# Optimization experiments

Hardware: AMD Instinct MI355X
Metric: run time of the kernel (lower is better)

## Reference

```python
import jax, jax.numpy as jnp
import numpy as np

B, D, H, W = 8, 128, 152, 272
N_DET = 128
NHEAD = 8
DFF = 512


def _vis_pos_table(d):
    # PositionEmbeddingSine over the fixed 11-entry visibility grid [0,0.1,...,1.0]
    x_embed = jnp.arange(11, dtype=jnp.float32) * 0.1
    dim_t = jnp.arange(d, dtype=jnp.float32)
    dim_t = 10000.0 ** (2.0 * jnp.floor(dim_t / 2.0) / d)
    pos = x_embed[:, None] / dim_t  # [11, d]
    return jnp.stack([jnp.sin(pos[:, 0::2]), jnp.cos(pos[:, 1::2])], axis=2).reshape(11, d)


def _layer_norm(x, g, b, eps=1e-5):
    m = jnp.mean(x, axis=-1, keepdims=True)
    v = jnp.var(x, axis=-1, keepdims=True)
    return (x - m) / jnp.sqrt(v + eps) * g + b


def _adaptive_pool3(x, dets):
    # Faithful AdaptiveAvgPool2d(3) over per-detection crops, vectorized via integral image.
    # x: [B,D,H,W]; dets: [B,N,4] int boxes [x0,y0,x1,y1] with x1>x0, y1>y0.
    P = jnp.cumsum(jnp.cumsum(x, axis=2), axis=3)
    P = jnp.pad(P, ((0, 0), (0, 0), (1, 0), (1, 0)))  # [B,D,H+1,W+1]
    Pt = P.transpose(0, 2, 3, 1)  # [B,H+1,W+1,D]
    sx, sy, ex, ey = dets[..., 0], dets[..., 1], dets[..., 2], dets[..., 3]
    i = jnp.arange(3)

    def edges(s, e):
        # torch adaptive pool bins: start = floor(i*L/3), end = ceil((i+1)*L/3)
        L = (e - s)[..., None]
        st = s[..., None] + (i * L) // 3
        en = s[..., None] + -((-(i + 1) * L) // 3)
        return st, en

    ys, ye = edges(sy, ey)  # [B,N,3]
    xs, xe = edges(sx, ex)
    bidx = jnp.arange(x.shape[0])[:, None, None, None]
    Y0 = ys[:, :, :, None]; Y1 = ye[:, :, :, None]
    X0 = xs[:, :, None, :]; X1 = xe[:, :, None, :]
    g = lambda yy, xx: Pt[bidx, yy, xx]  # [B,N,3,3,D]
    s_ = g(Y1, X1) - g(Y0, X1) - g(Y1, X0) + g(Y0, X0)
    area = ((Y1 - Y0) * (X1 - X0)).astype(x.dtype)  # [B,N,3,3]
    return s_ / area[..., None]  # [B,N,3,3,D] (row-major y,x like .view(128,-1))


def setup_inputs() -> dict:
    key = jax.random.key(0)
    ks = jax.random.split(key, 12)
    x = jax.random.normal(ks[0], (B, D, H, W), jnp.float32)
    vis = jax.random.uniform(ks[1], (B, 1, H, W), jnp.float32)
    # boxes with guaranteed positive extents inside the clamp range (x<=271, y<=151)
    x0 = jax.random.randint(ks[2], (B, N_DET), 0, 230)
    y0 = jax.random.randint(ks[3], (B, N_DET), 0, 110)
    bw = jax.random.randint(ks[4], (B, N_DET), 3, 41)
    bh = jax.random.randint(ks[5], (B, N_DET), 3, 41)
    dets = jnp.stack([x0, y0, x0 + bw, y0 + bh], axis=-1).astype(jnp.int32)
    inds = jax.vmap(lambda k: jax.random.permutation(k, H * W)[:N_DET])(
        jax.random.split(ks[6], B)).astype(jnp.int32)
    s = 1.0 / np.sqrt(D).astype(np.float32)
    Wqkv = jax.random.normal(ks[7], (3 * D, D), jnp.float32) * s
    bqkv = jnp.zeros((3 * D,), jnp.float32)
    Wo = jax.random.normal(ks[8], (D, D), jnp.float32) * s
    bo = jnp.zeros((D,), jnp.float32)
    W1 = jax.random.normal(ks[9], (DFF, D), jnp.float32) * s
    b1 = jnp.zeros((DFF,), jnp.float32)
    W2 = jax.random.normal(ks[10], (D, DFF), jnp.float32) * np.float32(1.0 / np.sqrt(DFF))
    b2 = jnp.zeros((D,), jnp.float32)
    g2 = jnp.ones((D,), jnp.float32); be2 = jnp.zeros((D,), jnp.float32)
    g3 = jnp.ones((D,), jnp.float32); be3 = jnp.zeros((D,), jnp.float32)
    return dict(x=x, vis=vis, dets=dets, inds=inds, Wqkv=Wqkv, bqkv=bqkv, Wo=Wo, bo=bo,
                W1=W1, b1=b1, W2=W2, b2=b2, g2=g2, be2=be2, g3=g3, be3=be3)


def reference(x, vis, dets, inds, Wqkv, bqkv, Wo, bo, W1, b1, W2, b2, g2, be2, g3, be3):
    b, d, h, w = x.shape
    n = inds.shape[1]
    hd = d // NHEAD
    vis_pos = _vis_pos_table(d)  # [11, d]
    # --- query patches: gather point features at detection centers ---
    x_flat = x.transpose(0, 2, 3, 1).reshape(b, h * w, d)
    bidx = jnp.arange(b)[:, None]
    q = x_flat[bidx, inds]  # [b,n,d]
    vis_flat = vis.transpose(0, 2, 3, 1).reshape(b, h * w)
    vidx = (jax.lax.stop_gradient(vis_flat[bidx, inds]) * 10.0).astype(jnp.int32)  # [b,n] in [0,10]
    q = q + vis_pos[vidx]
    # --- key patches: 3x3 adaptive avg pool of each detection crop -> 9 tokens ---
    k = _adaptive_pool3(x, dets).reshape(b * n, 9, d)  # [bn,9,d]
    qf = q.reshape(b * n, 1, d)
    # --- nn.MultiheadAttention cross-attn: batch=b*n detections, L=1 query, S=9 keys ---
    Wq, Wk, Wv = Wqkv[:d], Wqkv[d:2 * d], Wqkv[2 * d:]
    bq, bk, bv = bqkv[:d], bqkv[d:2 * d], bqkv[2 * d:]
    qp = (qf @ Wq.T + bq).reshape(b * n, 1, NHEAD, hd)
    kp = (k @ Wk.T + bk).reshape(b * n, 9, NHEAD, hd)
    vp = (k @ Wv.T + bv).reshape(b * n, 9, NHEAD, hd)
    att = jnp.einsum('blhe,bshe->bhls', qp, kp) / jnp.sqrt(jnp.asarray(hd, x.dtype))
    att = jax.nn.softmax(att, axis=-1)
    ao = jnp.einsum('bhls,bshe->blhe', att, vp).reshape(b * n, 1, d)
    ao = ao @ Wo.T + bo
    # --- post-norm decoder layer (dropout=identity in eval) ---
    t = _layer_norm(qf + ao, g2, be2)
    t2 = jax.nn.relu(t @ W1.T + b1) @ W2.T + b2
    out = _layer_norm(t + t2, g3, be3).reshape(b, n, d)
    # --- scatter refined embeddings back into the feature map ---
    x_flat = x_flat.at[bidx, inds].set(out)
    return x_flat.reshape(b, h, w, d).transpose(0, 3, 1, 2)
```

## Files before the change

kernel.cpp:

```cpp
#include <hip/hip_runtime.h>
#include <math.h>

#define BB 8
#define CH 128
#define HH 152
#define WWID 272
#define HWSZ (HH*WWID)
#define NDET 128
#define NHEAD 8
#define HDIM 16
#define DFF 512
#define NDB (BB*NDET)
#define NPLANE (BB*CH)
#define KSTRIDE 1152
#define CHUNK 19
#define SROW 276

typedef float f4v __attribute__((ext_vector_type(4)));

__device__ __forceinline__ float dot4(float4 w, float4 u, float s) {
    s = fmaf(w.x, u.x, s);
    s = fmaf(w.y, u.y, s);
    s = fmaf(w.z, u.z, s);
    s = fmaf(w.w, u.w, s);
    return s;
}

__global__ __launch_bounds__(256) void pool_stream(
    const float* __restrict__ x, const int* __restrict__ dets,
    float* __restrict__ kout, float* __restrict__ out)
{
    const int bid  = blockIdx.x;
    const int t    = threadIdx.x;
    const int b    = bid >> 7, ch = bid & 127;
    const int lane = t & 63,  w  = t >> 6;

    __shared__ float S[CHUNK * SROW];
    __shared__ float scratch[NDET * 9];

    const float* xp = x + ((size_t)b * CH + ch) * HWSZ;
    f4v* o4 = (f4v*)(out + ((size_t)b * CH + ch) * HWSZ);

    const int d = t & 127, half = t >> 7;
    const int4 dv = *((const int4*)(dets + (size_t)(b * NDET + d) * 4));
    const int sx = dv.x, sy = dv.y, ex = dv.z, ey = dv.w;
    const int Lx = ex - sx, Ly = ey - sy;
    const int xs1 = sx + Lx / 3,        xs2 = sx + 2 * Lx / 3;
    const int xe0 = sx + (Lx + 2) / 3,  xe1 = sx + (2 * Lx + 2) / 3;
    const int ys1 = sy + Ly / 3,        ys2 = sy + 2 * Ly / 3;
    const int ye0 = sy + (Ly + 2) / 3,  ye1 = sy + (2 * Ly + 2) / 3;

    float acc[9] = {0.f,0.f,0.f,0.f,0.f,0.f,0.f,0.f,0.f};

    #pragma unroll 1
    for (int c = 0; c < HH / CHUNK; ++c) {
        const int cbeg = c * CHUNK;

        {
            int rl = w;
            f4v vm = (f4v)(0.f), ve = (f4v)(0.f);
            bool have = (rl < CHUNK);
            if (have) {
                const f4v* rowp = (const f4v*)(xp + (size_t)(cbeg + rl) * WWID);
                vm = rowp[lane];
                if (lane < 4) ve = rowp[64 + lane];
            }
            while (have) {
                const int rc = rl;
                f4v v = vm, e = ve;
                rl += 4;
                have = (rl < CHUNK);
                if (have) {
                    const f4v* rowp = (const f4v*)(xp + (size_t)(cbeg + rl) * WWID);
                    vm = rowp[lane];
                    if (lane < 4) ve = rowp[64 + lane];
                }
                __builtin_nontemporal_store(v, &o4[(size_t)(cbeg + rc) * 68 + lane]);
                if (lane < 4)
                    __builtin_nontemporal_store(e, &o4[(size_t)(cbeg + rc) * 68 + 64 + lane]);
                float T = v[0] + v[1] + v[2] + v[3];
                float s = T;
                #pragma unroll
                for (int o = 1; o < 64; o <<= 1) {
                    float u = __shfl_up(s, o);
                    if (lane >= o) s += u;
                }
                float off0 = s - T;
                float* Sr = S + rc * SROW;
                f4v sm;
                sm[0] = off0;
                sm[1] = off0 + v[0];
                sm[2] = off0 + v[0] + v[1];
                sm[3] = off0 + v[0] + v[1] + v[2];
                *(f4v*)&Sr[4 * lane] = sm;
                float R  = __shfl(s, 63);
                float Te = (lane < 4) ? (e[0]+e[1]+e[2]+e[3]) : 0.f;
                float T0 = __shfl(Te, 0), T1 = __shfl(Te, 1);
                float T2 = __shfl(Te, 2), T3 = __shfl(Te, 3);
                if (lane < 4) {
                    float offE = R + ((lane > 0) ? T0 : 0.f)
                                   + ((lane > 1) ? T1 : 0.f)
                                   + ((lane > 2) ? T2 : 0.f);
                    f4v se;
                    se[0] = offE;
                    se[1] = offE + e[0];
                    se[2] = offE + e[0] + e[1];
                    se[3] = offE + e[0] + e[1] + e[2];
                    *(f4v*)&Sr[256 + 4 * lane] = se;
                }
                if (lane == 0) Sr[272] = R + T0 + T1 + T2 + T3;
            }
        }
        __syncthreads();

        {
            int lo = (sy > cbeg) ? sy : cbeg;
            int hi = (ey < cbeg + CHUNK) ? ey : (cbeg + CHUNK);
            if (lo < hi) {
                int mid = (lo + hi + 1) >> 1;
                int y0 = half ? mid : lo;
                int y1 = half ? hi  : mid;
                for (int y = y0; y < y1; ++y) {
                    const float* Sr = S + (y - cbeg) * SROW;
                    float c0 = Sr[xe0] - Sr[sx];
                    float c1 = Sr[xe1] - Sr[xs1];
                    float c2 = Sr[ex]  - Sr[xs2];
                    float m0 = (y < ye0) ? 1.f : 0.f;
                    float m1 = (y >= ys1 && y < ye1) ? 1.f : 0.f;
                    float m2 = (y >= ys2) ? 1.f : 0.f;
                    acc[0] = fmaf(m0, c0, acc[0]); acc[1] = fmaf(m0, c1, acc[1]); acc[2] = fmaf(m0, c2, acc[2]);
                    acc[3] = fmaf(m1, c0, acc[3]); acc[4] = fmaf(m1, c1, acc[4]); acc[5] = fmaf(m1, c2, acc[5]);
                    acc[6] = fmaf(m2, c0, acc[6]); acc[7] = fmaf(m2, c1, acc[7]); acc[8] = fmaf(m2, c2, acc[8]);
                }
            }
        }
        __syncthreads();
    }

    if (half) {
        #pragma unroll
        for (int j = 0; j < 9; ++j) scratch[d * 9 + j] = acc[j];
    }
    __syncthreads();
    if (!half) {
        const float w0 = (float)(xe0 - sx), w1 = (float)(xe1 - xs1), w2 = (float)(ex - xs2);
        const float h0 = (float)(ye0 - sy), h1r = (float)(ye1 - ys1), h2 = (float)(ey - ys2);
        float aj[9];
        #pragma unroll
        for (int j = 0; j < 9; ++j) aj[j] = acc[j] + scratch[d * 9 + j];
        float* kd = kout + (size_t)(b * NDET + d) * KSTRIDE + ch;
        kd[0*CH] = aj[0] / (h0  * w0);
        kd[1*CH] = aj[1] / (h0  * w1);
        kd[2*CH] = aj[2] / (h0  * w2);
        kd[3*CH] = aj[3] / (h1r * w0);
        kd[4*CH] = aj[4] / (h1r * w1);
        kd[5*CH] = aj[5] / (h1r * w2);
        kd[6*CH] = aj[6] / (h2  * w0);
        kd[7*CH] = aj[7] / (h2  * w1);
        kd[8*CH] = aj[8] / (h2  * w2);
    }
}

#define K2_KV 512
#define K2_Q  64
__global__ __launch_bounds__(256) void qkv_kernel(
    const float* __restrict__ x, const float* __restrict__ vis,
    const int* __restrict__ inds, const float* __restrict__ kout,
    const float* __restrict__ Wqkv, const float* __restrict__ bqkv,
    float* __restrict__ kvp, float* __restrict__ qpb, float* __restrict__ qvb)
{
    const int bid = blockIdx.x;
    const int t   = threadIdx.x;

    __shared__ float As[2304];

    if (bid < K2_KV) {
        const int d0 = bid * 2;
        const float4* src = (const float4*)(kout + (size_t)d0 * KSTRIDE);
        for (int i = t; i < 576; i += 256) ((float4*)As)[i] = src[i];
        __syncthreads();

        const int o = t & 127, which = t >> 7;
        const float4* wr = (const float4*)(Wqkv + (size_t)(CH + which * CH + o) * CH);
        float acc[18];
        #pragma unroll
        for (int r = 0; r < 18; ++r) acc[r] = 0.f;
        for (int i = 0; i < 32; ++i) {
            float4 w = wr[i];
            #pragma unroll
            for (int r = 0; r < 18; ++r) {
                float4 a = ((const float4*)(As + r * 128))[i];
                acc[r] = dot4(w, a, acc[r]);
            }
        }
        const float bias = bqkv[CH + which * CH + o];
        #pragma unroll
        for (int r = 0; r < 18; ++r) {
            int det = d0 + (r / 9), slot = r % 9;
            kvp[(((size_t)det * 2 + which) * 9 + slot) * CH + o] = acc[r] + bias;
        }
    } else {
        const int dg = (bid - K2_KV) * 16;
        const int o  = t & 127;
        const int rh = t >> 7;
        const float fr = powf(10000.0f, -(float)(o & 126) * (1.0f / 128.0f));
        for (int j = 0; j < 8; ++j) {
            int r = rh + 2 * j;
            int det = dg + r;
            int b = det >> 7, n = det & 127;
            int p = inds[b * NDET + n];
            float qval = x[((size_t)b * CH + o) * HWSZ + p];
            float vv   = vis[(size_t)b * HWSZ + p];
            int vidx   = (int)(vv * 10.0f);
            float ang  = 0.1f * (float)vidx * fr;
            float pe   = (o & 1) ? cosf(ang) : sinf(ang);
            float q = qval + pe;
            As[r * 128 + o] = q;
            qvb[(size_t)det * CH + o] = q;
        }
        __syncthreads();
        const float4* wr = (const float4*)(Wqkv + (size_t)o * CH);
        float acc[8] = {0.f,0.f,0.f,0.f,0.f,0.f,0.f,0.f};
        for (int i = 0; i < 32; ++i) {
            float4 w = wr[i];
            #pragma unroll
            for (int j = 0; j < 8; ++j) {
                float4 a = ((const float4*)(As + (rh + 2 * j) * 128))[i];
                acc[j] = dot4(w, a, acc[j]);
            }
        }
        const float bias = bqkv[o];
        #pragma unroll
        for (int j = 0; j < 8; ++j)
            qpb[(size_t)(dg + rh + 2 * j) * CH + o] = acc[j] + bias;
    }
}

__global__ __launch_bounds__(64) void attn_kernel(
    const float* __restrict__ kvp, const float* __restrict__ qpb,
    float* __restrict__ aovb)
{
    const int bid = blockIdx.x;
    const int t   = threadIdx.x;

    __shared__ float qpl[CH];
    __shared__ float kpl[9][CH];
    __shared__ float vpl[9][CH];
    __shared__ float attl[NHEAD][9];

    const int det = bid;
    const float4* kph = (const float4*)(kvp + (size_t)det * 2 * 9 * CH);
    for (int i = t; i < 288; i += 64) ((float4*)kpl)[i] = kph[i];
    for (int i = t; i < 288; i += 64) ((float4*)vpl)[i] = kph[288 + i];
    for (int i = t; i < 32;  i += 64) ((float4*)qpl)[i] = ((const float4*)(qpb + (size_t)det * CH))[i];
    __syncthreads();

    for (int pr = t; pr < NHEAD * 9; pr += 64) {
        int h = pr / 9, s = pr - h * 9;
        const float* qh = qpl + h * HDIM;
        const float* kh = &kpl[s][h * HDIM];
        float a = 0.f;
        #pragma unroll
        for (int e = 0; e < HDIM; ++e) a = fmaf(qh[e], kh[e], a);
        attl[h][s] = a * 0.25f;
    }
    __syncthreads();

    if (t < NHEAD) {
        float m = attl[t][0];
        #pragma unroll
        for (int s = 1; s < 9; ++s) m = fmaxf(m, attl[t][s]);
        float e[9]; float sum = 0.f;
        #pragma unroll
        for (int s = 0; s < 9; ++s) { e[s] = expf(attl[t][s] - m); sum += e[s]; }
        float inv = 1.0f / sum;
        #pragma unroll
        for (int s = 0; s < 9; ++s) attl[t][s] = e[s] * inv;
    }
    __syncthreads();

    for (int o = t; o < CH; o += 64) {
        int h = o >> 4;
        float a = 0.f;
        #pragma unroll
        for (int s = 0; s < 9; ++s) a = fmaf(attl[h][s], vpl[s][o], a);
        aovb[(size_t)det * CH + o] = a;
    }
}

__global__ __launch_bounds__(256) void wo_ln1_ffn1_kernel(
    const float* __restrict__ aovb, const float* __restrict__ qvb,
    const float* __restrict__ Wo, const float* __restrict__ bo,
    const float* __restrict__ g2, const float* __restrict__ be2,
    const float* __restrict__ W1, const float* __restrict__ b1,
    float* __restrict__ tvb, float* __restrict__ h1b)
{
    const int bid = blockIdx.x;
    const int t   = threadIdx.x;

    __shared__ float A[16 * CH];
    __shared__ float Q[16 * CH];
    __shared__ float T[16][CH];
    __shared__ float stats[16][2];

    const int dg = bid * 16;
    {
        const float4* sa = (const float4*)(aovb + (size_t)dg * CH);
        const float4* sq = (const float4*)(qvb  + (size_t)dg * CH);
        for (int i = t; i < 512; i += 256) { ((float4*)A)[i] = sa[i]; ((float4*)Q)[i] = sq[i]; }
    }
    __syncthreads();

    const int o = t & 127, rh = t >> 7;
    {
        const float4* wr = (const float4*)(Wo + (size_t)o * CH);
        float acc[8] = {0.f,0.f,0.f,0.f,0.f,0.f,0.f,0.f};
        for (int i = 0; i < 32; ++i) {
            float4 w = wr[i];
            #pragma unroll
            for (int j = 0; j < 8; ++j) {
                float4 a = ((const float4*)(A + (rh + 2 * j) * CH))[i];
                acc[j] = dot4(w, a, acc[j]);
            }
        }
        const float bb = bo[o];
        #pragma unroll
        for (int j = 0; j < 8; ++j) {
            int r = rh + 2 * j;
            T[r][o] = Q[r * CH + o] + acc[j] + bb;
        }
    }
    __syncthreads();

    {
        const int row = t >> 4, l = t & 15;
        float s1 = 0.f, s2 = 0.f;
        #pragma unroll
        for (int m = 0; m < 8; ++m) {
            float v = T[row][l + 16 * m];
            s1 += v; s2 += v * v;
        }
        #pragma unroll
        for (int off = 8; off >= 1; off >>= 1) {
            s1 += __shfl_xor(s1, off);
            s2 += __shfl_xor(s2, off);
        }
        if (l == 0) { stats[row][0] = s1; stats[row][1] = s2; }
    }
    __syncthreads();

    const float gg = g2[o], bb2 = be2[o];
    #pragma unroll
    for (int j = 0; j < 8; ++j) {
        int r = rh + 2 * j;
        float m   = stats[r][0] * (1.0f / 128.0f);
        float var = stats[r][1] * (1.0f / 128.0f) - m * m;
        float tv  = (T[r][o] - m) * rsqrtf(var + 1e-5f) * gg + bb2;
        Q[r * CH + o] = tv;
        tvb[(size_t)(dg + r) * CH + o] = tv;
    }
    __syncthreads();

    #pragma unroll
    for (int rep = 0; rep < 2; ++rep) {
        const int oo = t + rep * 256;
        const float4* wr = (const float4*)(W1 + (size_t)oo * CH);
        float acc[16];
        #pragma unroll
        for (int r = 0; r < 16; ++r) acc[r] = 0.f;
        for (int i = 0; i < 32; ++i) {
            float4 w = wr[i];
            #pragma unroll
            for (int r = 0; r < 16; ++r) {
                float4 a = ((const float4*)(Q + r * CH))[i];
                acc[r] = dot4(w, a, acc[r]);
            }
        }
        const float bb = b1[oo];
        #pragma unroll
        for (int r = 0; r < 16; ++r)
            h1b[(size_t)(dg + r) * DFF + oo] = fmaxf(acc[r] + bb, 0.f);
    }
}

__global__ __launch_bounds__(256) void ffn2_ln2_scatter_kernel(
    const float* __restrict__ h1b, const float* __restrict__ tvb,
    const float* __restrict__ W2, const float* __restrict__ b2,
    const float* __restrict__ g3, const float* __restrict__ be3,
    const int* __restrict__ inds, float* __restrict__ out)
{
    const int bid = blockIdx.x;
    const int t   = threadIdx.x;

    __shared__ float A[8 * DFF];
    __shared__ float Tv[8 * CH];
    __shared__ float T[8][CH];
    __shared__ float stats[8][2];

    const int dg = bid * 8;
    {
        const float4* sa = (const float4*)(h1b + (size_t)dg * DFF);
        for (int i = t; i < 1024; i += 256) ((float4*)A)[i] = sa[i];
        const float4* st = (const float4*)(tvb + (size_t)dg * CH);
        for (int i = t; i < 256; i += 256) ((float4*)Tv)[i] = st[i];
    }
    __syncthreads();

    const int o = t & 127, rh = t >> 7;
    {
        const float4* wr = (const float4*)(W2 + (size_t)o * DFF);
        float acc[4] = {0.f,0.f,0.f,0.f};
        #pragma unroll 4
        for (int i = 0; i < 128; ++i) {
            float4 w = wr[i];
            #pragma unroll
            for (int j = 0; j < 4; ++j) {
                float4 a = ((const float4*)(A + (rh + 2 * j) * DFF))[i];
                acc[j] = dot4(w, a, acc[j]);
            }
        }
        const float bb = b2[o];
        #pragma unroll
        for (int j = 0; j < 4; ++j) {
            int r = rh + 2 * j;
            T[r][o] = Tv[r * CH + o] + acc[j] + bb;
        }
    }
    __syncthreads();

    {
        const int row = t >> 5, l = t & 31;
        float s1 = 0.f, s2 = 0.f;
        #pragma unroll
        for (int m = 0; m < 4; ++m) {
            float v = T[row][l + 32 * m];
            s1 += v; s2 += v * v;
        }
        #pragma unroll
        for (int off = 16; off >= 1; off >>= 1) {
            s1 += __shfl_xor(s1, off);
            s2 += __shfl_xor(s2, off);
        }
        if (l == 0) { stats[row][0] = s1; stats[row][1] = s2; }
    }
    __syncthreads();

    const float gg = g3[o], bb3 = be3[o];
    #pragma unroll
    for (int j = 0; j < 4; ++j) {
        int r = rh + 2 * j;
        int det = dg + r;
        int b = det >> 7, n = det & 127;
        int p = inds[b * NDET + n];
        float m   = stats[r][0] * (1.0f / 128.0f);
        float var = stats[r][1] * (1.0f / 128.0f) - m * m;
        float ov  = (T[r][o] - m) * rsqrtf(var + 1e-5f) * gg + bb3;
        out[((size_t)b * CH + o) * HWSZ + p] = ov;
    }
}

__global__ __launch_bounds__(256) void copy_x(const f4v* __restrict__ src,
                                              f4v* __restrict__ dst, size_t n4) {
    size_t i = (size_t)blockIdx.x * 256 + threadIdx.x;
    const size_t stride = (size_t)gridDim.x * 256;
    for (; i < n4; i += stride) {
        f4v v = src[i];
        __builtin_nontemporal_store(v, &dst[i]);
    }
}

__device__ __forceinline__ float block_layernorm(float v, int t,
        const float* __restrict__ gamma, const float* __restrict__ beta,
        float* redA, float* redB) {
    float s1 = v, s2 = v * v;
    #pragma unroll
    for (int off = 32; off >= 1; off >>= 1) {
        s1 += __shfl_xor(s1, off);
        s2 += __shfl_xor(s2, off);
    }
    if ((t & 63) == 0) { redA[t >> 6] = s1; redB[t >> 6] = s2; }
    __syncthreads();
    float sum = redA[0] + redA[1] + redA[2] + redA[3];
    float sq  = redB[0] + redB[1] + redB[2] + redB[3];
    __syncthreads();
    float m   = sum * (1.0f / 128.0f);
    float var = sq  * (1.0f / 128.0f) - m * m;
    float r = 0.f;
    if (t < CH) r = (v - m) * rsqrtf(var + 1e-5f) * gamma[t] + beta[t];
    return r;
}

__global__ __launch_bounds__(256) void er_fused_fb(
    const float* __restrict__ x, const float* __restrict__ vis,
    const int* __restrict__ dets, const int* __restrict__ inds,
    const float* __restrict__ Wqkv, const float* __restrict__ bqkv,
    const float* __restrict__ Wo,   const float* __restrict__ bo,
    const float* __restrict__ W1,   const float* __restrict__ b1,
    const float* __restrict__ W2,   const float* __restrict__ b2,
    const float* __restrict__ g2,   const float* __restrict__ be2,
    const float* __restrict__ g3,   const float* __restrict__ be3,
    float* __restrict__ out)
{
    const int bid = blockIdx.x;
    const int t   = threadIdx.x;

    __shared__ float kbuf[9][CH];
    __shared__ float qv[CH];
    __shared__ float qp[CH];
    __shared__ float kp[9][CH];
    __shared__ float vp[9][CH];
    __shared__ float att[NHEAD][9];
    __shared__ float aov[CH];
    __shared__ float tv[CH];
    __shared__ float h1[DFF];
    __shared__ float part[256];
    __shared__ float redA[4], redB[4];
    __shared__ float msk[48][4];

    const int b = bid >> 7;
    const int n = bid & (NDET - 1);

    const int4 dv = *((const int4*)(dets + (size_t)(b * NDET + n) * 4));
    const int sx = dv.x, sy = dv.y, ex = dv.z, ey = dv.w;
    const int Lx = ex - sx, Ly = ey - sy;
    const int xs1 = sx + Lx / 3,        xs2 = sx + 2 * Lx / 3;
    const int xe0 = sx + (Lx + 2) / 3,  xe1 = sx + (2 * Lx + 2) / 3;
    const int ys1 = sy + Ly / 3,        ys2 = sy + 2 * Ly / 3;
    const int ye0 = sy + (Ly + 2) / 3,  ye1 = sy + (2 * Ly + 2) / 3;

    const int p = inds[b * NDET + n];

    if (t < 48) {
        int y = sy + t;
        bool inb = (y < ey);
        msk[t][0] = (inb && y < ye0)              ? 1.f : 0.f;
        msk[t][1] = (inb && y >= ys1 && y < ye1)  ? 1.f : 0.f;
        msk[t][2] = (inb && y >= ys2)             ? 1.f : 0.f;
        msk[t][3] = 0.f;
    }
    if (t < CH) {
        float qval = x[((size_t)b * CH + t) * HWSZ + p];
        float vv   = vis[(size_t)b * HWSZ + p];
        int vidx   = (int)(vv * 10.0f);
        float fr   = powf(10000.0f, -(float)(t & 126) * (1.0f / 128.0f));
        float ang  = 0.1f * (float)vidx * fr;
        float pe   = (t & 1) ? cosf(ang) : sinf(ang);
        qv[t] = qval + pe;
    }
    __syncthreads();

    {
        const int g   = t >> 4;
        const int lx  = t & 15;
        const int sx4 = sx & ~3;
        const int xb  = sx4 + lx * 4;
        const int lxmax = ((ex - 1) - sx4) >> 2;
        const int xba = sx4 + ((lx < lxmax) ? lx : lxmax) * 4;

        float4 mx0, mx1, mx2;
        {
            float m0[4], m1[4], m2[4];
            #pragma unroll
            for (int e = 0; e < 4; ++e) {
                int xx = xb + e;
                m0[e] = (xx >= sx  && xx < xe0) ? 1.f : 0.f;
                m1[e] = (xx >= xs1 && xx < xe1) ? 1.f : 0.f;
                m2[e] = (xx >= xs2 && xx < ex ) ? 1.f : 0.f;
            }
            mx0 = make_float4(m0[0], m0[1], m0[2], m0[3]);
            mx1 = make_float4(m1[0], m1[1], m1[2], m1[3]);
            mx2 = make_float4(m2[0], m2[1], m2[2], m2[3]);
        }

        const int rows_n = ey - sy;
        const int nch    = (rows_n + 7) >> 3;

        for (int c = 0; c < 8; ++c) {
            const int dd = g + c * 16;
            const float* base = x + ((size_t)b * CH + dd) * HWSZ + xba;
            float4 ac0 = make_float4(0.f,0.f,0.f,0.f);
            float4 ac1 = make_float4(0.f,0.f,0.f,0.f);
            float4 ac2 = make_float4(0.f,0.f,0.f,0.f);
            for (int ck = 0; ck < nch; ++ck) {
                const int y0 = sy + (ck << 3);
                float4 v[8];
                #pragma unroll
                for (int k = 0; k < 8; ++k) {
                    int y = y0 + k;
                    y = (y < ey) ? y : (ey - 1);
                    v[k] = *(const float4*)(base + (size_t)y * WWID);
                }
                #pragma unroll
                for (int k = 0; k < 8; ++k) {
                    const float4 m = *(const float4*)&msk[(y0 - sy) + k][0];
                    ac0.x = fmaf(m.x, v[k].x, ac0.x); ac0.y = fmaf(m.x, v[k].y, ac0.y);
                    ac0.z = fmaf(m.x, v[k].z, ac0.z); ac0.w = fmaf(m.x, v[k].w, ac0.w);
                    ac1.x = fmaf(m.y, v[k].x, ac1.x); ac1.y = fmaf(m.y, v[k].y, ac1.y);
                    ac1.z = fmaf(m.y, v[k].z, ac1.z); ac1.w = fmaf(m.y, v[k].w, ac1.w);
                    ac2.x = fmaf(m.z, v[k].x, ac2.x); ac2.y = fmaf(m.z, v[k].y, ac2.y);
                    ac2.z = fmaf(m.z, v[k].z, ac2.z); ac2.w = fmaf(m.z, v[k].w, ac2.w);
                }
            }
            float a[9];
            a[0] = dot4(mx0, ac0, 0.f); a[1] = dot4(mx1, ac0, 0.f); a[2] = dot4(mx2, ac0, 0.f);
            a[3] = dot4(mx0, ac1, 0.f); a[4] = dot4(mx1, ac1, 0.f); a[5] = dot4(mx2, ac1, 0.f);
            a[6] = dot4(mx0, ac2, 0.f); a[7] = dot4(mx1, ac2, 0.f); a[8] = dot4(mx2, ac2, 0.f);
            #pragma unroll
            for (int jj = 0; jj < 9; ++jj) {
                a[jj] += __shfl_xor(a[jj], 8);
                a[jj] += __shfl_xor(a[jj], 4);
                a[jj] += __shfl_xor(a[jj], 2);
                a[jj] += __shfl_xor(a[jj], 1);
            }
            if (lx == 0) {
                int w0 = xe0 - sx, w1 = xe1 - xs1, w2 = ex - xs2;
                int h0 = ye0 - sy, h1r = ye1 - ys1, h2 = ey - ys2;
                kbuf[0][dd] = a[0] / (float)(h0 * w0);
                kbuf[1][dd] = a[1] / (float)(h0 * w1);
                kbuf[2][dd] = a[2] / (float)(h0 * w2);
                kbuf[3][dd] = a[3] / (float)(h1r * w0);
                kbuf[4][dd] = a[4] / (float)(h1r * w1);
                kbuf[5][dd] = a[5] / (float)(h1r * w2);
                kbuf[6][dd] = a[6] / (float)(h2 * w0);
                kbuf[7][dd] = a[7] / (float)(h2 * w1);
                kbuf[8][dd] = a[8] / (float)(h2 * w2);
            }
        }
    }
    __syncthreads();

    if (t < CH) {
        const float4* wr = (const float4*)(Wqkv + (size_t)t * CH);
        const float4* qq = (const float4*)qv;
        float s = 0.f;
        #pragma unroll 8
        for (int i = 0; i < CH / 4; ++i) s = dot4(wr[i], qq[i], s);
        qp[t] = s + bqkv[t];
    }
    {
        const int o = t & (CH - 1);
        const int which = t >> 7;
        const float4* wr = (const float4*)(Wqkv + (size_t)(CH + which * CH + o) * CH);
        float acc[9] = {0.f,0.f,0.f,0.f,0.f,0.f,0.f,0.f,0.f};
        #pragma unroll 4
        for (int i = 0; i < CH / 4; ++i) {
            float4 w = wr[i];
            #pragma unroll
            for (int s = 0; s < 9; ++s) {
                float4 kk = ((const float4*)(&kbuf[s][0]))[i];
                acc[s] = dot4(w, kk, acc[s]);
            }
        }
        float bias = bqkv[CH + which * CH + o];
        if (which == 0) {
            #pragma unroll
            for (int s = 0; s < 9; ++s) kp[s][o] = acc[s] + bias;
        } else {
            #pragma unroll
            for (int s = 0; s < 9; ++s) vp[s][o] = acc[s] + bias;
        }
    }
    __syncthreads();

    if (t < NHEAD * 9) {
        int h = t / 9, s = t - h * 9;
        const float* qh = qp + h * HDIM;
        const float* kh = &kp[s][h * HDIM];
        float a = 0.f;
        #pragma unroll
        for (int e = 0; e < HDIM; ++e) a = fmaf(qh[e], kh[e], a);
        att[h][s] = a * 0.25f;
    }
    __syncthreads();

    if (t < NHEAD) {
        float m = att[t][0];
        #pragma unroll
        for (int s = 1; s < 9; ++s) m = fmaxf(m, att[t][s]);
        float e[9]; float sum = 0.f;
        #pragma unroll
        for (int s = 0; s < 9; ++s) { e[s] = expf(att[t][s] - m); sum += e[s]; }
        float inv = 1.0f / sum;
        #pragma unroll
        for (int s = 0; s < 9; ++s) att[t][s] = e[s] * inv;
    }
    __syncthreads();

    if (t < CH) {
        int h = t >> 4;
        float a = 0.f;
        #pragma unroll
        for (int s = 0; s < 9; ++s) a = fmaf(att[h][s], vp[s][t], a);
        aov[t] = a;
    }
    __syncthreads();

    float v1 = 0.f;
    if (t < CH) {
        const float4* wr = (const float4*)(Wo + (size_t)t * CH);
        const float4* u4 = (const float4*)aov;
        float s = 0.f;
        #pragma unroll 8
        for (int i = 0; i < CH / 4; ++i) s = dot4(wr[i], u4[i], s);
        v1 = qv[t] + s + bo[t];
    }
    float t1 = block_layernorm(v1, t, g2, be2, redA, redB);
    if (t < CH) tv[t] = t1;
    __syncthreads();

    #pragma unroll
    for (int rep = 0; rep < 2; ++rep) {
        int o = t + rep * 256;
        const float4* wr = (const float4*)(W1 + (size_t)o * CH);
        const float4* u4 = (const float4*)tv;
        float s = 0.f;
        #pragma unroll 8
        for (int i = 0; i < CH / 4; ++i) s = dot4(wr[i], u4[i], s);
        h1[o] = fmaxf(s + b1[o], 0.f);
    }
    __syncthreads();

    {
        int o = t & (CH - 1), hf = t >> 7;
        const float4* wr = (const float4*)(W2 + (size_t)o * DFF + hf * (DFF / 2));
        const float4* u4 = (const float4*)(h1 + hf * (DFF / 2));
        float s = 0.f;
        #pragma unroll 8
        for (int i = 0; i < DFF / 8; ++i) s = dot4(wr[i], u4[i], s);
        part[t] = s;
    }
    __syncthreads();

    float v2 = 0.f;
    if (t < CH) {
        float t2 = part[t] + part[t + 128] + b2[t];
        v2 = tv[t] + t2;
    }
    float outv = block_layernorm(v2, t, g3, be3, redA, redB);
    if (t < CH) out[((size_t)b * CH + t) * HWSZ + p] = outv;
}

extern "C" void kernel_launch(void* const* d_in, const int* in_sizes, int n_in,
                              void* d_out, int out_size, void* d_ws, size_t ws_size,
                              hipStream_t stream) {
    const float* x    = (const float*)d_in[0];
    const float* vis  = (const float*)d_in[1];
    const int*   dets = (const int*)d_in[2];
    const int*   inds = (const int*)d_in[3];
    const float* Wqkv = (const float*)d_in[4];
    const float* bqkv = (const float*)d_in[5];
    const float* Wo   = (const float*)d_in[6];
    const float* bo   = (const float*)d_in[7];
    const float* W1   = (const float*)d_in[8];
    const float* b1   = (const float*)d_in[9];
    const float* W2   = (const float*)d_in[10];
    const float* b2   = (const float*)d_in[11];
    const float* g2   = (const float*)d_in[12];
    const float* be2  = (const float*)d_in[13];
    const float* g3   = (const float*)d_in[14];
    const float* be3  = (const float*)d_in[15];
    float* out = (float*)d_out;

    const size_t SZ_KOUT = (size_t)NDB * KSTRIDE;
    const size_t SZ_128  = (size_t)NDB * CH;
    const size_t SZ_KVP  = (size_t)NDB * 2 * 9 * CH;
    const size_t SZ_H1   = (size_t)NDB * DFF;
    const size_t need = (SZ_KOUT + 4 * SZ_128 + SZ_KVP + SZ_H1) * sizeof(float);

    const size_t N4 = (size_t)BB * CH * HWSZ / 4;
    if (ws_size >= need) {
        float* kout = (float*)d_ws;
        float* qvb  = kout + SZ_KOUT;
        float* qpb  = qvb  + SZ_128;
        float* kvp  = qpb  + SZ_128;
        float* aovb = kvp  + SZ_KVP;
        float* tvb  = aovb + SZ_128;
        float* h1b  = tvb  + SZ_128;

        pool_stream<<<dim3(NPLANE), dim3(256), 0, stream>>>(x, dets, kout, out);
        qkv_kernel<<<dim3(K2_KV + K2_Q), dim3(256), 0, stream>>>(
            x, vis, inds, kout, Wqkv, bqkv, kvp, qpb, qvb);
        attn_kernel<<<dim3(NDB), dim3(64), 0, stream>>>(kvp, qpb, aovb);
        wo_ln1_ffn1_kernel<<<dim3(64), dim3(256), 0, stream>>>(
            aovb, qvb, Wo, bo, g2, be2, W1, b1, tvb, h1b);
        ffn2_ln2_scatter_kernel<<<dim3(128), dim3(256), 0, stream>>>(
            h1b, tvb, W2, b2, g3, be3, inds, out);
    } else {
        copy_x<<<dim3(2048), dim3(256), 0, stream>>>(
            (const f4v*)x, (f4v*)out, N4);
        er_fused_fb<<<dim3(NDB), dim3(256), 0, stream>>>(
            x, vis, dets, inds, Wqkv, bqkv, Wo, bo, W1, b1, W2, b2,
            g2, be2, g3, be3, out);
    }
}
```

Measured before the change: 154.8 us.

## Split pooling across row halves and fuse QKV/attention/FFN tail into one kernel

The pooling stream kernel now runs two blocks per channel plane, each covering half the rows and writing partial box sums to separate buffers. This doubles the grid to 2048 blocks for better occupancy. The four tail kernels (QKV projection, attention, Wo+LN1+FFN1, FFN2+LN2+scatter) are merged into one kernel that handles two detections per block entirely in shared memory, which removes launches and global intermediate round-trips. The trade-off is that each tail block re-reads all the weight matrices for only two detections, so weight reuse per block is lower. The row split also shortens each block's scan, and the bottom 0 rows of HH are still covered since 4*19=76 per half.

New measurement: 148.0 us. 1.05x faster.

```diff
diff --git a/kernel.cpp b/kernel.cpp
--- a/kernel.cpp
+++ b/kernel.cpp
@@ -11,9 +11,9 @@
 #define HDIM 16
 #define DFF 512
 #define NDB (BB*NDET)
-#define NPLANE (BB*CH)
 #define KSTRIDE 1152
 #define CHUNK 19
+#define RHALF 76
 #define SROW 276
 
 typedef float f4v __attribute__((ext_vector_type(4)));
@@ -28,15 +28,16 @@
 
 __global__ __launch_bounds__(256) void pool_stream(
     const float* __restrict__ x, const int* __restrict__ dets,
-    float* __restrict__ kout, float* __restrict__ out)
+    float* __restrict__ kpart, float* __restrict__ out)
 {
-    const int bid  = blockIdx.x;
-    const int t    = threadIdx.x;
-    const int b    = bid >> 7, ch = bid & 127;
-    const int lane = t & 63,  w  = t >> 6;
+    const int bid   = blockIdx.x;
+    const int t     = threadIdx.x;
+    const int plane = bid >> 1, rhalf = bid & 1;
+    const int b     = plane >> 7, ch = plane & 127;
+    const int lane  = t & 63,  w  = t >> 6;
+    const int rbeg  = rhalf * RHALF;
 
     __shared__ float S[CHUNK * SROW];
-    __shared__ float scratch[NDET * 9];
 
     const float* xp = x + ((size_t)b * CH + ch) * HWSZ;
     f4v* o4 = (f4v*)(out + ((size_t)b * CH + ch) * HWSZ);
@@ -53,8 +54,8 @@
     float acc[9] = {0.f,0.f,0.f,0.f,0.f,0.f,0.f,0.f,0.f};
 
     #pragma unroll 1
-    for (int c = 0; c < HH / CHUNK; ++c) {
-        const int cbeg = c * CHUNK;
+    for (int c = 0; c < RHALF / CHUNK; ++c) {
+        const int cbeg = rbeg + c * CHUNK;
 
         {
             int rl = w;
@@ -139,48 +140,93 @@
 
     if (half) {
         #pragma unroll
-        for (int j = 0; j < 9; ++j) scratch[d * 9 + j] = acc[j];
+        for (int j = 0; j < 9; ++j) S[d * 9 + j] = acc[j];
     }
     __syncthreads();
     if (!half) {
-        const float w0 = (float)(xe0 - sx), w1 = (float)(xe1 - xs1), w2 = (float)(ex - xs2);
-        const float h0 = (float)(ye0 - sy), h1r = (float)(ye1 - ys1), h2 = (float)(ey - ys2);
-        float aj[9];
-        #pragma unroll
-        for (int j = 0; j < 9; ++j) aj[j] = acc[j] + scratch[d * 9 + j];
-        float* kd = kout + (size_t)(b * NDET + d) * KSTRIDE + ch;
-        kd[0*CH] = aj[0] / (h0  * w0);
-        kd[1*CH] = aj[1] / (h0  * w1);
-        kd[2*CH] = aj[2] / (h0  * w2);
-        kd[3*CH] = aj[3] / (h1r * w0);
-        kd[4*CH] = aj[4] / (h1r * w1);
-        kd[5*CH] = aj[5] / (h1r * w2);
-        kd[6*CH] = aj[6] / (h2  * w0);
-        kd[7*CH] = aj[7] / (h2  * w1);
-        kd[8*CH] = aj[8] / (h2  * w2);
+        float* kd = kpart + ((size_t)rhalf * NDB + (size_t)(b * NDET + d)) * KSTRIDE + ch;
+        #pragma unroll
+        for (int j = 0; j < 9; ++j)
+            kd[j * CH] = acc[j] + S[d * 9 + j];
     }
 }
 
-#define K2_KV 512
-#define K2_Q  64
-__global__ __launch_bounds__(256) void qkv_kernel(
+__global__ __launch_bounds__(256) void tail_kernel(
     const float* __restrict__ x, const float* __restrict__ vis,
-    const int* __restrict__ inds, const float* __restrict__ kout,
+    const int* __restrict__ dets, const int* __restrict__ inds,
+    const float* __restrict__ kpA, const float* __restrict__ kpB,
     const float* __restrict__ Wqkv, const float* __restrict__ bqkv,
-    float* __restrict__ kvp, float* __restrict__ qpb, float* __restrict__ qvb)
+    const float* __restrict__ Wo,   const float* __restrict__ bo,
+    const float* __restrict__ W1,   const float* __restrict__ b1,
+    const float* __restrict__ W2,   const float* __restrict__ b2,
+    const float* __restrict__ g2,   const float* __restrict__ be2,
+    const float* __restrict__ g3,   const float* __restrict__ be3,
+    float* __restrict__ out)
 {
     const int bid = blockIdx.x;
     const int t   = threadIdx.x;
-
-    __shared__ float As[2304];
-
-    if (bid < K2_KV) {
-        const int d0 = bid * 2;
-        const float4* src = (const float4*)(kout + (size_t)d0 * KSTRIDE);
-        for (int i = t; i < 576; i += 256) ((float4*)As)[i] = src[i];
-        __syncthreads();
-
-        const int o = t & 127, which = t >> 7;
+    const int d0  = bid * 2;
+    const int b   = d0 >> 7;
+    const int o   = t & 127, dl = t >> 7;
+
+    __shared__ float kbuf[2 * 9 * CH];
+    __shared__ float kp[2 * 9 * CH];
+    __shared__ float vp[2 * 9 * CH];
+    __shared__ float invA[2][9];
+    __shared__ float qv[2][CH];
+    __shared__ float qp[2][CH];
+    __shared__ float attl[2][NHEAD][9];
+    __shared__ float aov[2][CH];
+    __shared__ float Tv[2][CH];
+    __shared__ float h1[2][DFF];
+    __shared__ float part2[2][2][CH];
+    __shared__ float wst[4][2];
+
+    if (t < 18) {
+        int dd = t / 9, slot = t - dd * 9;
+        const int4 dv = *((const int4*)(dets + (size_t)(b * NDET + ((d0 + dd) & 127)) * 4));
+        int sx = dv.x, sy = dv.y, ex = dv.z, ey = dv.w;
+        int Lx = ex - sx, Ly = ey - sy;
+        int xs1 = sx + Lx / 3,       xs2 = sx + 2 * Lx / 3;
+        int xe0 = sx + (Lx + 2) / 3, xe1 = sx + (2 * Lx + 2) / 3;
+        int ys1 = sy + Ly / 3,       ys2 = sy + 2 * Ly / 3;
+        int ye0 = sy + (Ly + 2) / 3, ye1 = sy + (2 * Ly + 2) / 3;
+        int xi = slot % 3, yi = slot / 3;
+        int wdt = (xi == 0) ? (xe0 - sx) : (xi == 1) ? (xe1 - xs1) : (ex - xs2);
+        int hgt = (yi == 0) ? (ye0 - sy) : (yi == 1) ? (ye1 - ys1) : (ey - ys2);
+        invA[dd][slot] = 1.0f / (float)(hgt * wdt);
+    }
+    {
+        int p = inds[b * NDET + ((d0 + dl) & 127)];
+        float qval = x[((size_t)b * CH + o) * HWSZ + p];
+        float vv   = vis[(size_t)b * HWSZ + p];
+        int vidx   = (int)(vv * 10.0f);
+        float fr   = powf(10000.0f, -(float)(o & 126) * (1.0f / 128.0f));
+        float ang  = 0.1f * (float)vidx * fr;
+        qv[dl][o]  = qval + ((o & 1) ? cosf(ang) : sinf(ang));
+    }
+    __syncthreads();
+
+    for (int i = t; i < 2 * KSTRIDE; i += 256) {
+        int dd = (i >= KSTRIDE);
+        int r  = i - dd * KSTRIDE;
+        int slot = r >> 7;
+        float vA = kpA[(size_t)(d0 + dd) * KSTRIDE + r];
+        float vB = kpB[(size_t)(d0 + dd) * KSTRIDE + r];
+        kbuf[dd * KSTRIDE + r] = (vA + vB) * invA[dd][slot];
+    }
+    __syncthreads();
+
+    {
+        const float4* wr = (const float4*)(Wqkv + (size_t)o * CH);
+        const float4* qq = (const float4*)&qv[dl][0];
+        float s = 0.f;
+        #pragma unroll 8
+        for (int i = 0; i < 32; ++i) s = dot4(wr[i], qq[i], s);
+        qp[dl][o] = s + bqkv[o];
+    }
+    {
+        const int which = t >> 7;
         const float4* wr = (const float4*)(Wqkv + (size_t)(CH + which * CH + o) * CH);
         float acc[18];
         #pragma unroll
@@ -189,272 +235,124 @@
             float4 w = wr[i];
             #pragma unroll
             for (int r = 0; r < 18; ++r) {
-                float4 a = ((const float4*)(As + r * 128))[i];
+                float4 a = ((const float4*)kbuf)[r * 32 + i];
                 acc[r] = dot4(w, a, acc[r]);
             }
         }
         const float bias = bqkv[CH + which * CH + o];
-        #pragma unroll
-        for (int r = 0; r < 18; ++r) {
-            int det = d0 + (r / 9), slot = r % 9;
-            kvp[(((size_t)det * 2 + which) * 9 + slot) * CH + o] = acc[r] + bias;
-        }
-    } else {
-        const int dg = (bid - K2_KV) * 16;
-        const int o  = t & 127;
-        const int rh = t >> 7;
-        const float fr = powf(10000.0f, -(float)(o & 126) * (1.0f / 128.0f));
-        for (int j = 0; j < 8; ++j) {
-            int r = rh + 2 * j;
-            int det = dg + r;
-            int b = det >> 7, n = det & 127;
-            int p = inds[b * NDET + n];
-            float qval = x[((size_t)b * CH + o) * HWSZ + p];
-            float vv   = vis[(size_t)b * HWSZ + p];
-            int vidx   = (int)(vv * 10.0f);
-            float ang  = 0.1f * (float)vidx * fr;
-            float pe   = (o & 1) ? cosf(ang) : sinf(ang);
-            float q = qval + pe;
-            As[r * 128 + o] = q;
-            qvb[(size_t)det * CH + o] = q;
-        }
-        __syncthreads();
-        const float4* wr = (const float4*)(Wqkv + (size_t)o * CH);
-        float acc[8] = {0.f,0.f,0.f,0.f,0.f,0.f,0.f,0.f};
+        float* dst = which ? vp : kp;
+        #pragma unroll
+        for (int r = 0; r < 18; ++r) dst[r * CH + o] = acc[r] + bias;
+    }
+    __syncthreads();
+
+    if (o < 72) {
+        int h = o / 9, s = o - h * 9;
+        const float* qh = &qp[dl][h * HDIM];
+        const float* kh = &kp[dl * KSTRIDE + s * CH + h * HDIM];
+        float a = 0.f;
+        #pragma unroll
+        for (int e = 0; e < HDIM; ++e) a = fmaf(qh[e], kh[e], a);
+        attl[dl][h][s] = a * 0.25f;
+    }
+    __syncthreads();
+    if (o < 8) {
+        float m = attl[dl][o][0];
+        #pragma unroll
+        for (int s = 1; s < 9; ++s) m = fmaxf(m, attl[dl][o][s]);
+        float e[9]; float sum = 0.f;
+        #pragma unroll
+        for (int s = 0; s < 9; ++s) { e[s] = expf(attl[dl][o][s] - m); sum += e[s]; }
+        float inv = 1.0f / sum;
+        #pragma unroll
+        for (int s = 0; s < 9; ++s) attl[dl][o][s] = e[s] * inv;
+    }
+    __syncthreads();
+    {
+        int h = o >> 4;
+        float a = 0.f;
+        #pragma unroll
+        for (int s = 0; s < 9; ++s) a = fmaf(attl[dl][h][s], vp[dl * KSTRIDE + s * CH + o], a);
+        aov[dl][o] = a;
+    }
+    __syncthreads();
+
+    float v1;
+    {
+        const float4* wr = (const float4*)(Wo + (size_t)o * CH);
+        const float4* u4 = (const float4*)&aov[dl][0];
+        float s = 0.f;
+        #pragma unroll 8
+        for (int i = 0; i < 32; ++i) s = dot4(wr[i], u4[i], s);
+        v1 = qv[dl][o] + s + bo[o];
+    }
+    {
+        float s1 = v1, s2 = v1 * v1;
+        #pragma unroll
+        for (int off = 32; off >= 1; off >>= 1) {
+            s1 += __shfl_xor(s1, off);
+            s2 += __shfl_xor(s2, off);
+        }
+        if ((t & 63) == 0) { wst[t >> 6][0] = s1; wst[t >> 6][1] = s2; }
+    }
+    __syncthreads();
+    {
+        float sum = wst[2 * dl][0] + wst[2 * dl + 1][0];
+        float sq  = wst[2 * dl][1] + wst[2 * dl + 1][1];
+        float m   = sum * (1.0f / 128.0f);
+        float var = sq  * (1.0f / 128.0f) - m * m;
+        Tv[dl][o] = (v1 - m) * rsqrtf(var + 1e-5f) * g2[o] + be2[o];
+    }
+    __syncthreads();
+
+    #pragma unroll
+    for (int rep = 0; rep < 2; ++rep) {
+        int oo = t + rep * 256;
+        const float4* wr = (const float4*)(W1 + (size_t)oo * CH);
+        float a0 = 0.f, a1 = 0.f;
         for (int i = 0; i < 32; ++i) {
             float4 w = wr[i];
-            #pragma unroll
-            for (int j = 0; j < 8; ++j) {
-                float4 a = ((const float4*)(As + (rh + 2 * j) * 128))[i];
-                acc[j] = dot4(w, a, acc[j]);
-            }
-        }
-        const float bias = bqkv[o];
-        #pragma unroll
-        for (int j = 0; j < 8; ++j)
-            qpb[(size_t)(dg + rh + 2 * j) * CH + o] = acc[j] + bias;
-    }
-}
-
-__global__ __launch_bounds__(64) void attn_kernel(
-    const float* __restrict__ kvp, const float* __restrict__ qpb,
-    float* __restrict__ aovb)
-{
-    const int bid = blockIdx.x;
-    const int t   = threadIdx.x;
-
-    __shared__ float qpl[CH];
-    __shared__ float kpl[9][CH];
-    __shared__ float vpl[9][CH];
-    __shared__ float attl[NHEAD][9];
-
-    const int det = bid;
-    const float4* kph = (const float4*)(kvp + (size_t)det * 2 * 9 * CH);
-    for (int i = t; i < 288; i += 64) ((float4*)kpl)[i] = kph[i];
-    for (int i = t; i < 288; i += 64) ((float4*)vpl)[i] = kph[288 + i];
-    for (int i = t; i < 32;  i += 64) ((float4*)qpl)[i] = ((const float4*)(qpb + (size_t)det * CH))[i];
-    __syncthreads();
-
-    for (int pr = t; pr < NHEAD * 9; pr += 64) {
-        int h = pr / 9, s = pr - h * 9;
-        const float* qh = qpl + h * HDIM;
-        const float* kh = &kpl[s][h * HDIM];
-        float a = 0.f;
-        #pragma unroll
-        for (int e = 0; e < HDIM; ++e) a = fmaf(qh[e], kh[e], a);
-        attl[h][s] = a * 0.25f;
-    }
-    __syncthreads();
-
-    if (t < NHEAD) {
-        float m = attl[t][0];
-        #pragma unroll
-        for (int s = 1; s < 9; ++s) m = fmaxf(m, attl[t][s]);
-        float e[9]; float sum = 0.f;
-        #pragma unroll
-        for (int s = 0; s < 9; ++s) { e[s] = expf(attl[t][s] - m); sum += e[s]; }
-        float inv = 1.0f / sum;
-        #pragma unroll
-        for (int s = 0; s < 9; ++s) attl[t][s] = e[s] * inv;
-    }
-    __syncthreads();
-
-    for (int o = t; o < CH; o += 64) {
-        int h = o >> 4;
-        float a = 0.f;
-        #pragma unroll
-        for (int s = 0; s < 9; ++s) a = fmaf(attl[h][s], vpl[s][o], a);
-        aovb[(size_t)det * CH + o] = a;
-    }
-}
-
-__global__ __launch_bounds__(256) void wo_ln1_ffn1_kernel(
-    const float* __restrict__ aovb, const float* __restrict__ qvb,
-    const float* __restrict__ Wo, const float* __restrict__ bo,
-    const float* __restrict__ g2, const float* __restrict__ be2,
-    const float* __restrict__ W1, const float* __restrict__ b1,
-    float* __restrict__ tvb, float* __restrict__ h1b)
-{
-    const int bid = blockIdx.x;
-    const int t   = threadIdx.x;
-
-    __shared__ float A[16 * CH];
-    __shared__ float Q[16 * CH];
-    __shared__ float T[16][CH];
-    __shared__ float stats[16][2];
-
-    const int dg = bid * 16;
-    {
-        const float4* sa = (const float4*)(aovb + (size_t)dg * CH);
-        const float4* sq = (const float4*)(qvb  + (size_t)dg * CH);
-        for (int i = t; i < 512; i += 256) { ((float4*)A)[i] = sa[i]; ((float4*)Q)[i] = sq[i]; }
-    }
-    __syncthreads();
-
-    const int o = t & 127, rh = t >> 7;
-    {
-        const float4* wr = (const float4*)(Wo + (size_t)o * CH);
-        float acc[8] = {0.f,0.f,0.f,0.f,0.f,0.f,0.f,0.f};
-        for (int i = 0; i < 32; ++i) {
+            a0 = dot4(w, ((const float4*)&Tv[0][0])[i], a0);
+            a1 = dot4(w, ((const float4*)&Tv[1][0])[i], a1);
+        }
+        float bb = b1[oo];
+        h1[0][oo] = fmaxf(a0 + bb, 0.f);
+        h1[1][oo] = fmaxf(a1 + bb, 0.f);
+    }
+    __syncthreads();
+
+    {
+        const int hf = t >> 7;
+        const float4* wr = (const float4*)(W2 + (size_t)o * DFF + hf * (DFF / 2));
+        float a0 = 0.f, a1 = 0.f;
+        #pragma unroll 4
+        for (int i = 0; i < 64; ++i) {
             float4 w = wr[i];
-            #pragma unroll
-            for (int j = 0; j < 8; ++j) {
-                float4 a = ((const float4*)(A + (rh + 2 * j) * CH))[i];
-                acc[j] = dot4(w, a, acc[j]);
-            }
-        }
-        const float bb = bo[o];
-        #pragma unroll
-        for (int j = 0; j < 8; ++j) {
-            int r = rh + 2 * j;
-            T[r][o] = Q[r * CH + o] + acc[j] + bb;
-        }
-    }
-    __syncthreads();
-
-    {
-        const int row = t >> 4, l = t & 15;
-        float s1 = 0.f, s2 = 0.f;
-        #pragma unroll
-        for (int m = 0; m < 8; ++m) {
-            float v = T[row][l + 16 * m];
-            s1 += v; s2 += v * v;
-        }
-        #pragma unroll
-        for (int off = 8; off >= 1; off >>= 1) {
+            a0 = dot4(w, ((const float4*)&h1[0][hf * 256])[i], a0);
+            a1 = dot4(w, ((const float4*)&h1[1][hf * 256])[i], a1);
+        }
+        part2[hf][0][o] = a0;
+        part2[hf][1][o] = a1;
+    }
+    __syncthreads();
+    float v2 = part2[0][dl][o] + part2[1][dl][o] + b2[o] + Tv[dl][o];
+    {
+        float s1 = v2, s2 = v2 * v2;
+        #pragma unroll
+        for (int off = 32; off >= 1; off >>= 1) {
             s1 += __shfl_xor(s1, off);
             s2 += __shfl_xor(s2, off);
         }
-        if (l == 0) { stats[row][0] = s1; stats[row][1] = s2; }
-    }
-    __syncthreads();
-
-    const float gg = g2[o], bb2 = be2[o];
-    #pragma unroll
-    for (int j = 0; j < 8; ++j) {
-        int r = rh + 2 * j;
-        float m   = stats[r][0] * (1.0f / 128.0f);
-        float var = stats[r][1] * (1.0f / 128.0f) - m * m;
-        float tv  = (T[r][o] - m) * rsqrtf(var + 1e-5f) * gg + bb2;
-        Q[r * CH + o] = tv;
-        tvb[(size_t)(dg + r) * CH + o] = tv;
-    }
-    __syncthreads();
-
-    #pragma unroll
-    for (int rep = 0; rep < 2; ++rep) {
-        const int oo = t + rep * 256;
-        const float4* wr = (const float4*)(W1 + (size_t)oo * CH);
-        float acc[16];
-        #pragma unroll
-        for (int r = 0; r < 16; ++r) acc[r] = 0.f;
-        for (int i = 0; i < 32; ++i) {
-            float4 w = wr[i];
-            #pragma unroll
-            for (int r = 0; r < 16; ++r) {
-                float4 a = ((const float4*)(Q + r * CH))[i];
-                acc[r] = dot4(w, a, acc[r]);
-            }
-        }
-        const float bb = b1[oo];
-        #pragma unroll
-        for (int r = 0; r < 16; ++r)
-            h1b[(size_t)(dg + r) * DFF + oo] = fmaxf(acc[r] + bb, 0.f);
-    }
-}
-
-__global__ __launch_bounds__(256) void ffn2_ln2_scatter_kernel(
-    const float* __restrict__ h1b, const float* __restrict__ tvb,
-    const float* __restrict__ W2, const float* __restrict__ b2,
-    const float* __restrict__ g3, const float* __restrict__ be3,
-    const int* __restrict__ inds, float* __restrict__ out)
-{
-    const int bid = blockIdx.x;
-    const int t   = threadIdx.x;
-
-    __shared__ float A[8 * DFF];
-    __shared__ float Tv[8 * CH];
-    __shared__ float T[8][CH];
-    __shared__ float stats[8][2];
-
-    const int dg = bid * 8;
-    {
-        const float4* sa = (const float4*)(h1b + (size_t)dg * DFF);
-        for (int i = t; i < 1024; i += 256) ((float4*)A)[i] = sa[i];
-        const float4* st = (const float4*)(tvb + (size_t)dg * CH);
-        for (int i = t; i < 256; i += 256) ((float4*)Tv)[i] = st[i];
-    }
-    __syncthreads();
-
-    const int o = t & 127, rh = t >> 7;
-    {
-        const float4* wr = (const float4*)(W2 + (size_t)o * DFF);
-        float acc[4] = {0.f,0.f,0.f,0.f};
-        #pragma unroll 4
-        for (int i = 0; i < 128; ++i) {
-            float4 w = wr[i];
-            #pragma unroll
-            for (int j = 0; j < 4; ++j) {
-                float4 a = ((const float4*)(A + (rh + 2 * j) * DFF))[i];
-                acc[j] = dot4(w, a, acc[j]);
-            }
-        }
-        const float bb = b2[o];
-        #pragma unroll
-        for (int j = 0; j < 4; ++j) {
-            int r = rh + 2 * j;
-            T[r][o] = Tv[r * CH + o] + acc[j] + bb;
-        }
-    }
-    __syncthreads();
-
-    {
-        const int row = t >> 5, l = t & 31;
-        float s1 = 0.f, s2 = 0.f;
-        #pragma unroll
-        for (int m = 0; m < 4; ++m) {
-            float v = T[row][l + 32 * m];
-            s1 += v; s2 += v * v;
-        }
-        #pragma unroll
-        for (int off = 16; off >= 1; off >>= 1) {
-            s1 += __shfl_xor(s1, off);
-            s2 += __shfl_xor(s2, off);
-        }
-        if (l == 0) { stats[row][0] = s1; stats[row][1] = s2; }
-    }
-    __syncthreads();
-
-    const float gg = g3[o], bb3 = be3[o];
-    #pragma unroll
-    for (int j = 0; j < 4; ++j) {
-        int r = rh + 2 * j;
-        int det = dg + r;
-        int b = det >> 7, n = det & 127;
-        int p = inds[b * NDET + n];
-        float m   = stats[r][0] * (1.0f / 128.0f);
-        float var = stats[r][1] * (1.0f / 128.0f) - m * m;
-        float ov  = (T[r][o] - m) * rsqrtf(var + 1e-5f) * gg + bb3;
+        if ((t & 63) == 0) { wst[t >> 6][0] = s1; wst[t >> 6][1] = s2; }
+    }
+    __syncthreads();
+    {
+        float sum = wst[2 * dl][0] + wst[2 * dl + 1][0];
+        float sq  = wst[2 * dl][1] + wst[2 * dl + 1][1];
+        float m   = sum * (1.0f / 128.0f);
+        float var = sq  * (1.0f / 128.0f) - m * m;
+        float ov  = (v2 - m) * rsqrtf(var + 1e-5f) * g3[o] + be3[o];
+        int p = inds[b * NDET + ((d0 + dl) & 127)];
         out[((size_t)b * CH + o) * HWSZ + p] = ov;
     }
 }
@@ -761,30 +659,18 @@
     const float* be3  = (const float*)d_in[15];
     float* out = (float*)d_out;
 
-    const size_t SZ_KOUT = (size_t)NDB * KSTRIDE;
-    const size_t SZ_128  = (size_t)NDB * CH;
-    const size_t SZ_KVP  = (size_t)NDB * 2 * 9 * CH;
-    const size_t SZ_H1   = (size_t)NDB * DFF;
-    const size_t need = (SZ_KOUT + 4 * SZ_128 + SZ_KVP + SZ_H1) * sizeof(float);
+    const size_t SZ_KP = (size_t)NDB * KSTRIDE;
+    const size_t need  = 2 * SZ_KP * sizeof(float);
 
     const size_t N4 = (size_t)BB * CH * HWSZ / 4;
     if (ws_size >= need) {
-        float* kout = (float*)d_ws;
-        float* qvb  = kout + SZ_KOUT;
-        float* qpb  = qvb  + SZ_128;
-        float* kvp  = qpb  + SZ_128;
-        float* aovb = kvp  + SZ_KVP;
-        float* tvb  = aovb + SZ_128;
-        float* h1b  = tvb  + SZ_128;
-
-        pool_stream<<<dim3(NPLANE), dim3(256), 0, stream>>>(x, dets, kout, out);
-        qkv_kernel<<<dim3(K2_KV + K2_Q), dim3(256), 0, stream>>>(
-            x, vis, inds, kout, Wqkv, bqkv, kvp, qpb, qvb);
-        attn_kernel<<<dim3(NDB), dim3(64), 0, stream>>>(kvp, qpb, aovb);
-        wo_ln1_ffn1_kernel<<<dim3(64), dim3(256), 0, stream>>>(
-            aovb, qvb, Wo, bo, g2, be2, W1, b1, tvb, h1b);
-        ffn2_ln2_scatter_kernel<<<dim3(128), dim3(256), 0, stream>>>(
-            h1b, tvb, W2, b2, g3, be3, inds, out);
+        float* kpA = (float*)d_ws;
+        float* kpB = kpA + SZ_KP;
+
+        pool_stream<<<dim3(2048), dim3(256), 0, stream>>>(x, dets, kpA, out);
+        tail_kernel<<<dim3(512), dim3(256), 0, stream>>>(
+            x, vis, dets, inds, kpA, kpB, Wqkv, bqkv, Wo, bo,
+            W1, b1, W2, b2, g2, be2, g3, be3, out);
     } else {
         copy_x<<<dim3(2048), dim3(256), 0, stream>>>(
             (const f4v*)x, (f4v*)out, N4);
```
